# Kernel optimization log

Measured on AMD Instinct MI355X. Metric: run time of the kernel, lower is better.

## Reference

```python
import jax, jax.numpy as jnp
import numpy as np

N, CIN, NU = 8192, 4096, 4096

def setup_inputs() -> dict:
    key = jax.random.key(0)
    k1, k2, k3 = jax.random.split(key, 3)
    x = jax.random.normal(k1, (N, CIN), dtype=jnp.float32)
    W = jax.random.normal(k2, (CIN, NU), dtype=jnp.float32)
    b = jax.random.normal(k3, (NU,), dtype=jnp.float32)
    return {"x": x, "W": W, "b": b}

def reference(x, W, b):
    # binary_weight: sign-binarize to {+1,-1} (sign(0) -> +1)
    bw = jnp.where(W >= 0, jnp.float32(1.0), jnp.float32(-1.0))
    out = jnp.matmul(x, bw) + b  # [N, n_units]
    return jax.nn.relu(out)
```

## Files before the change

kernel.cpp:

```cpp
#include <hip/hip_runtime.h>


typedef __attribute__((ext_vector_type(8))) __bf16 bf16x8;
typedef __attribute__((ext_vector_type(4))) float f32x4;

#define BM 128
#define BN 128
#define BK 32

__device__ __forceinline__ unsigned int bf_pack(unsigned int lo, unsigned int hi) {
    unsigned int l = (lo + 0x7FFFu + ((lo >> 16) & 1u)) >> 16;
    unsigned int h = (hi + 0x7FFFu + ((hi >> 16) & 1u)) >> 16;
    return l | (h << 16);
}

__global__ void cvt_x_kernel(const uint4* __restrict__ in, uint4* __restrict__ out, int nchunk) {
    int i = blockIdx.x * blockDim.x + threadIdx.x;
    int stride = gridDim.x * blockDim.x;
    for (; i < nchunk; i += stride) {
        uint4 a = in[2 * i];
        uint4 b = in[2 * i + 1];
        uint4 o;
        o.x = bf_pack(a.x, a.y);
        o.y = bf_pack(a.z, a.w);
        o.z = bf_pack(b.x, b.y);
        o.w = bf_pack(b.z, b.w);
        out[i] = o;
    }
}

__global__ void binT_kernel(const float* __restrict__ W, unsigned short* __restrict__ Wt,
                            int K, int N) {
    __shared__ unsigned short tile[32][33];
    int tx = threadIdx.x;
    int ty = threadIdx.y;
    int k0 = blockIdx.y * 32;
    int n0 = blockIdx.x * 32;
    #pragma unroll
    for (int i = 0; i < 32; i += 8) {
        unsigned int u = __float_as_uint(W[(size_t)(k0 + ty + i) * N + n0 + tx]);
        tile[ty + i][tx] = (unsigned short)(0x3F80u | ((u >> 16) & 0x8000u));
    }
    __syncthreads();
    #pragma unroll
    for (int i = 0; i < 32; i += 8) {
        Wt[(size_t)(n0 + ty + i) * K + k0 + tx] = tile[tx][ty + i];
    }
}

__global__ __launch_bounds__(256) void gemm_bin_kernel(
    const unsigned short* __restrict__ A,
    const unsigned short* __restrict__ Bt,
    const float* __restrict__ bias,
    float* __restrict__ C, int M, int N, int K)
{
    __shared__ unsigned short lda[BM * BK];
    __shared__ unsigned short ldb[BN * BK];

    const int t = threadIdx.x;
    const int w = t >> 6;
    const int l = t & 63;
    const int wm = w >> 1;
    const int wn = w & 1;
    const int lr = l & 15;
    const int lk = l >> 4;

    const int brow = blockIdx.y * BM;
    const int bcol = blockIdx.x * BN;

    f32x4 acc[4][4] = {};

    const int soff0 = w * 512 + l * 8;

    for (int k0 = 0; k0 < K; k0 += BK) {
        __syncthreads();
        #pragma unroll
        for (int r = 0; r < 2; ++r) {
            int off = r * 2048 + soff0;
            int row = off >> 5, col = off & 31;
            const unsigned short* gsrc = A + (size_t)(brow + row) * K + (k0 + col);
            __builtin_amdgcn_global_load_lds(
                (const __attribute__((address_space(1))) void*)gsrc,
                (__attribute__((address_space(3))) void*)&lda[r * 2048 + w * 512],
                16, 0, 0);
        }
        #pragma unroll
        for (int r = 0; r < 2; ++r) {
            int off = r * 2048 + soff0;
            int row = off >> 5, col = off & 31;
            const unsigned short* gsrc = Bt + (size_t)(bcol + row) * K + (k0 + col);
            __builtin_amdgcn_global_load_lds(
                (const __attribute__((address_space(1))) void*)gsrc,
                (__attribute__((address_space(3))) void*)&ldb[r * 2048 + w * 512],
                16, 0, 0);
        }
        __syncthreads();

        bf16x8 af[4], bfr[4];
        #pragma unroll
        for (int m = 0; m < 4; ++m) {
            int row = wm * 64 + m * 16 + lr;
            af[m] = *(const bf16x8*)&lda[row * BK + lk * 8];
        }
        #pragma unroll
        for (int n = 0; n < 4; ++n) {
            int col = wn * 64 + n * 16 + lr;
            bfr[n] = *(const bf16x8*)&ldb[col * BK + lk * 8];
        }
        #pragma unroll
        for (int m = 0; m < 4; ++m)
            #pragma unroll
            for (int n = 0; n < 4; ++n)
                acc[m][n] = __builtin_amdgcn_mfma_f32_16x16x32_bf16(
                    af[m], bfr[n], acc[m][n], 0, 0, 0);
    }

    #pragma unroll
    for (int n = 0; n < 4; ++n) {
        int col = bcol + wn * 64 + n * 16 + lr;
        float bv = bias[col];
        #pragma unroll
        for (int m = 0; m < 4; ++m) {
            #pragma unroll
            for (int j = 0; j < 4; ++j) {
                int row = brow + wm * 64 + m * 16 + lk * 4 + j;
                float v = acc[m][n][j] + bv;
                C[(size_t)row * N + col] = v > 0.f ? v : 0.f;
            }
        }
    }
}

extern "C" void kernel_launch(void* const* d_in, const int* in_sizes, int n_in,
                              void* d_out, int out_size, void* d_ws, size_t ws_size,
                              hipStream_t stream) {
    const float* x = (const float*)d_in[0];
    const float* W = (const float*)d_in[1];
    const float* b = (const float*)d_in[2];
    float* out = (float*)d_out;

    const int N = in_sizes[2];
    const int K = in_sizes[1] / N;
    const int M = in_sizes[0] / K;

    unsigned short* xb = (unsigned short*)d_ws;
    unsigned short* wt = xb + (size_t)M * K;

    int nchunk = (M * K) / 8;
    cvt_x_kernel<<<2048, 256, 0, stream>>>((const uint4*)x, (uint4*)xb, nchunk);

    binT_kernel<<<dim3(N / 32, K / 32), dim3(32, 8), 0, stream>>>(W, wt, K, N);

    gemm_bin_kernel<<<dim3(N / BN, M / BM), 256, 0, stream>>>(xb, wt, b, out, M, N, K);
}
```

Baseline: 600.1 us.

## Rewrite GEMM as 256x256 tile, 8-wave multi-stage pipelined kernel with swizzled LDS

Replaces the 128x128, single-buffered GEMM with a 256x256 tile, 512-thread kernel. Each k-step is split into phases that issue async global-to-LDS loads for future tiles while MFMAs run on the current ones, with explicit vmcnt waits, sched barriers and setprio. It also adds an XOR swizzle on LDS to avoid bank conflicts and remaps workgroups across XCDs for L2 locality. The cost is 128KB of LDS and a large accumulator register footprint, which limits occupancy, and a fragile hand-written wait schedule.

```diff
diff --git a/kernel.cpp b/kernel.cpp
--- a/kernel.cpp
+++ b/kernel.cpp
@@ -4,9 +4,26 @@
 typedef __attribute__((ext_vector_type(8))) __bf16 bf16x8;
 typedef __attribute__((ext_vector_type(4))) float f32x4;
 
-#define BM 128
-#define BN 128
-#define BK 32
+#define GBM 256
+#define GBN 256
+
+#define VMW(n) do { __builtin_amdgcn_sched_barrier(0); \
+    asm volatile("s_waitcnt vmcnt(" #n ")" ::: "memory"); \
+    __builtin_amdgcn_sched_barrier(0); } while (0)
+#define SB() do { __builtin_amdgcn_sched_barrier(0); \
+    __builtin_amdgcn_s_barrier(); \
+    __builtin_amdgcn_sched_barrier(0); } while (0)
+
+#define PH(buf, ks, mh, LB, STG, VN) \
+    ldA(buf, ks, mh); \
+    if (LB) ldB(buf, ks); \
+    STG; \
+    SB(); \
+    __builtin_amdgcn_s_setprio(1); \
+    mm(mh); \
+    __builtin_amdgcn_s_setprio(0); \
+    VMW(VN); \
+    SB();
 
 __device__ __forceinline__ unsigned int bf_pack(unsigned int lo, unsigned int hi) {
     unsigned int l = (lo + 0x7FFFu + ((lo >> 16) & 1u)) >> 16;
@@ -48,83 +65,120 @@
     }
 }
 
-__global__ __launch_bounds__(256) void gemm_bin_kernel(
+__global__ __launch_bounds__(512, 2) void gemm8_kernel(
     const unsigned short* __restrict__ A,
     const unsigned short* __restrict__ Bt,
     const float* __restrict__ bias,
-    float* __restrict__ C, int M, int N, int K)
+    float* __restrict__ C, int M, int N, int K, int nbx)
 {
-    __shared__ unsigned short lda[BM * BK];
-    __shared__ unsigned short ldb[BN * BK];
-
-    const int t = threadIdx.x;
-    const int w = t >> 6;
-    const int l = t & 63;
-    const int wm = w >> 1;
-    const int wn = w & 1;
-    const int lr = l & 15;
-    const int lk = l >> 4;
-
-    const int brow = blockIdx.y * BM;
-    const int bcol = blockIdx.x * BN;
-
-    f32x4 acc[4][4] = {};
-
-    const int soff0 = w * 512 + l * 8;
-
-    for (int k0 = 0; k0 < K; k0 += BK) {
-        __syncthreads();
-        #pragma unroll
-        for (int r = 0; r < 2; ++r) {
-            int off = r * 2048 + soff0;
-            int row = off >> 5, col = off & 31;
-            const unsigned short* gsrc = A + (size_t)(brow + row) * K + (k0 + col);
+    __shared__ __align__(16) unsigned short lds[65536];
+
+    const int tid = threadIdx.x;
+    const int w = tid >> 6, l = tid & 63;
+    const int wm = w >> 2, wn = w & 3;
+    const int lr = l & 15, lk = l >> 4;
+
+    const int cpx = gridDim.x >> 3;
+    const int wg = blockIdx.x;
+    const int swz = (wg & 7) * cpx + (wg >> 3);
+    const int bx = swz % nbx, by = swz / nbx;
+    const int brow = by * GBM, bcol = bx * GBN;
+
+    f32x4 acc[8][4] = {};
+
+    const int srow0 = w * 16 + (l >> 2);
+    const int koff = (((l & 3) ^ ((l >> 3) & 3)) << 3);
+    const unsigned short* aS[2] = {
+        A  + (size_t)(brow + srow0) * K + koff,
+        A  + (size_t)(brow + 128 + srow0) * K + koff };
+    const unsigned short* bS[2] = {
+        Bt + (size_t)(bcol + srow0) * K + koff,
+        Bt + (size_t)(bcol + 128 + srow0) * K + koff };
+
+    const int cswz = ((lk ^ ((lr >> 1) & 3)) << 3);
+    const int aOff = (wm * 128 + lr) * 32 + cswz;
+    const int bOff = (wn * 64 + lr) * 32 + cswz;
+
+    auto stA = [&](int t, int ks) {
+        int base = ((((t & 1) << 1) | ks) << 13) + w * 512;
+        int kg = t * 64 + ks * 32;
+        #pragma unroll
+        for (int j = 0; j < 2; ++j)
             __builtin_amdgcn_global_load_lds(
-                (const __attribute__((address_space(1))) void*)gsrc,
-                (__attribute__((address_space(3))) void*)&lda[r * 2048 + w * 512],
+                (const __attribute__((address_space(1))) void*)(aS[j] + kg),
+                (__attribute__((address_space(3))) void*)&lds[base + j * 4096],
                 16, 0, 0);
-        }
-        #pragma unroll
-        for (int r = 0; r < 2; ++r) {
-            int off = r * 2048 + soff0;
-            int row = off >> 5, col = off & 31;
-            const unsigned short* gsrc = Bt + (size_t)(bcol + row) * K + (k0 + col);
+    };
+    auto stB = [&](int t, int ks) {
+        int base = 32768 + ((((t & 1) << 1) | ks) << 13) + w * 512;
+        int kg = t * 64 + ks * 32;
+        #pragma unroll
+        for (int j = 0; j < 2; ++j)
             __builtin_amdgcn_global_load_lds(
-                (const __attribute__((address_space(1))) void*)gsrc,
-                (__attribute__((address_space(3))) void*)&ldb[r * 2048 + w * 512],
+                (const __attribute__((address_space(1))) void*)(bS[j] + kg),
+                (__attribute__((address_space(3))) void*)&lds[base + j * 4096],
                 16, 0, 0);
-        }
-        __syncthreads();
-
-        bf16x8 af[4], bfr[4];
-        #pragma unroll
-        for (int m = 0; m < 4; ++m) {
-            int row = wm * 64 + m * 16 + lr;
-            af[m] = *(const bf16x8*)&lda[row * BK + lk * 8];
-        }
-        #pragma unroll
-        for (int n = 0; n < 4; ++n) {
-            int col = wn * 64 + n * 16 + lr;
-            bfr[n] = *(const bf16x8*)&ldb[col * BK + lk * 8];
-        }
-        #pragma unroll
-        for (int m = 0; m < 4; ++m)
+    };
+
+    bf16x8 af[4], bf[4];
+    auto ldA = [&](int buf, int ks, int mh) {
+        int base = (((buf << 1) | ks) << 13) + mh * 64 * 32 + aOff;
+        #pragma unroll
+        for (int fm = 0; fm < 4; ++fm)
+            af[fm] = *(const bf16x8*)&lds[base + fm * 16 * 32];
+    };
+    auto ldB = [&](int buf, int ks) {
+        int base = 32768 + (((buf << 1) | ks) << 13) + bOff;
+        #pragma unroll
+        for (int fn = 0; fn < 4; ++fn)
+            bf[fn] = *(const bf16x8*)&lds[base + fn * 16 * 32];
+    };
+    auto mm = [&](int mh) {
+        #pragma unroll
+        for (int fm = 0; fm < 4; ++fm)
             #pragma unroll
-            for (int n = 0; n < 4; ++n)
-                acc[m][n] = __builtin_amdgcn_mfma_f32_16x16x32_bf16(
-                    af[m], bfr[n], acc[m][n], 0, 0, 0);
+            for (int fn = 0; fn < 4; ++fn)
+                acc[mh * 4 + fm][fn] = __builtin_amdgcn_mfma_f32_16x16x32_bf16(
+                    af[fm], bf[fn], acc[mh * 4 + fm][fn], 0, 0, 0);
+    };
+
+    stA(0, 0); stB(0, 0); stA(0, 1); stB(0, 1); stA(1, 0); stB(1, 0);
+    VMW(6); SB();
+
+    const int NI = K >> 7;
+    for (int i = 0; i < NI - 1; ++i) {
+        int t0 = 2 * i, t1 = t0 + 1;
+        PH(0, 0, 0, true,  stA(t1, 1),     6)
+        PH(0, 0, 1, false, stB(t1, 1),     6)
+        PH(0, 1, 1, true,  stA(t0 + 2, 0), 6)
+        PH(0, 1, 0, false, stB(t0 + 2, 0), 6)
+        PH(1, 0, 0, true,  stA(t0 + 2, 1), 6)
+        PH(1, 0, 1, false, stB(t0 + 2, 1), 6)
+        PH(1, 1, 1, true,  stA(t1 + 2, 0), 6)
+        PH(1, 1, 0, false, stB(t1 + 2, 0), 6)
+    }
+    {
+        int t1 = 2 * NI - 1;
+        PH(0, 0, 0, true,  stA(t1, 1), 6)
+        PH(0, 0, 1, false, stB(t1, 1), 6)
+        PH(0, 1, 1, true,  (void)0,    4)
+        PH(0, 1, 0, false, (void)0,    4)
+        PH(1, 0, 0, true,  (void)0,    2)
+        PH(1, 0, 1, false, (void)0,    0)
+        PH(1, 1, 1, true,  (void)0,    0)
+        PH(1, 1, 0, false, (void)0,    0)
     }
 
     #pragma unroll
-    for (int n = 0; n < 4; ++n) {
-        int col = bcol + wn * 64 + n * 16 + lr;
+    for (int fn = 0; fn < 4; ++fn) {
+        int col = bcol + wn * 64 + fn * 16 + lr;
         float bv = bias[col];
         #pragma unroll
-        for (int m = 0; m < 4; ++m) {
+        for (int im = 0; im < 8; ++im) {
             #pragma unroll
             for (int j = 0; j < 4; ++j) {
-                int row = brow + wm * 64 + m * 16 + lk * 4 + j;
-                float v = acc[m][n][j] + bv;
+                int row = brow + wm * 128 + im * 16 + lk * 4 + j;
+                float v = acc[im][fn][j] + bv;
                 C[(size_t)row * N + col] = v > 0.f ? v : 0.f;
             }
         }
@@ -151,5 +205,7 @@
 
     binT_kernel<<<dim3(N / 32, K / 32), dim3(32, 8), 0, stream>>>(W, wt, K, N);
 
-    gemm_bin_kernel<<<dim3(N / BN, M / BM), 256, 0, stream>>>(xb, wt, b, out, M, N, K);
-}
+    int nbx = N / GBN;
+    int nwg = (M / GBM) * nbx;
+    gemm8_kernel<<<nwg, 512, 0, stream>>>(xb, wt, b, out, M, N, K, nbx);
+}
```

Result: faster. 503.9 us (-16.0%).
